# Performance work log

Hardware: AMD Instinct MI355X
Metric: run time of the kernel (lower is better)

## Reference

```python
import jax, jax.numpy as jnp
import numpy as np


def setup_inputs() -> dict:
    key = jax.random.key(0)
    k1, k2, k3 = jax.random.split(key, 3)
    return {
        "x": jax.random.normal(k1, (1, 64, 28, 28), dtype=jnp.float32),
        "w1": jax.random.normal(k2, (128, 32, 3, 3, 2), dtype=jnp.float32),  # weights[0]
        "w2": jax.random.normal(k3, (64, 3, 2), dtype=jnp.float32),          # weights[1]
    }


def reference(x, w1, w2):
    # Stage 1: first unfold + einsum == depthwise size-3 conv along W (pad 1),
    # producing 2 taps (k) per channel.
    xr = x.reshape(64, 28, 28)                      # (j, m=H, n=W)
    xp = jnp.pad(xr, ((0, 0), (0, 0), (1, 1)))      # zero-pad W by 1
    # t3[j, m, i, n] = xp[j, m, n + i]  (i = kernel offset 0..2)
    t3 = jnp.stack([xp[:, :, i:i + 28] for i in range(3)], axis=2)  # (64,28,3,28)
    t4 = jnp.einsum('jmin,jik->jmnk', t3, w2)       # (64,28,28,2)

    # Stage 2: pairwise channel-sum 64 -> 32
    t5 = t4.reshape(32, 2, 28, 28, 2).sum(axis=1)   # (l=32, h=28, w=28, k=2)

    # Stage 3: the two remaining unfolds + final einsum == standard 3x3 conv,
    # pad 1, in_channels = (l,k) = 64, out_channels = 128.
    inp = jnp.transpose(t5, (0, 3, 1, 2)).reshape(1, 64, 28, 28)       # NCHW, C=(l,k)
    w = jnp.transpose(w1, (0, 1, 4, 2, 3)).reshape(128, 64, 3, 3)      # OIHW, I=(l,m)
    y = jax.lax.conv_general_dilated(
        inp, w, window_strides=(1, 1), padding=((1, 1), (1, 1)),
        dimension_numbers=('NCHW', 'OIHW', 'NCHW'))
    return y  # (1, 128, 28, 28)
```

## Files before the change

kernel.cpp:

```cpp
#include <hip/hip_runtime.h>
#include <hip/hip_bf16.h>

__global__ __launch_bounds__(256) void fused_kernel(
    const float* __restrict__ x,
    const float* __restrict__ w1,
    const float* __restrict__ w2,
    float* __restrict__ y)
{
    __shared__ __align__(16) float sA[64 * 6 * 36];
    __shared__ __align__(16) float sRed[256][4];

    const int b     = blockIdx.x;
    const int opair = b / 7;
    const int band  = b % 7;
    const int tid   = threadIdx.x;

    #pragma unroll
    for (int round = 0; round < 2; ++round) {
        int pair = tid + round * 256;
        if (pair < 384) {
            int c  = pair / 6;
            int pr = pair % 6;
            int m  = band * 4 + pr - 1;
            float* dst = &sA[pair * 36];
            if (m < 0 || m > 27) {
                #pragma unroll
                for (int t = 0; t < 15; ++t)
                    ((float2*)dst)[t] = make_float2(0.f, 0.f);
            } else {
                int j0 = c & ~1;
                int k  = c & 1;
                const float* xr0 = x + (j0 * 28 + m) * 28;
                const float* xr1 = xr0 + 28 * 28;
                const float* w2p = w2 + j0 * 6 + k;
                float wa0 = w2p[0], wa1 = w2p[2],  wa2 = w2p[4];
                float wb0 = w2p[6], wb1 = w2p[8],  wb2 = w2p[10];

                float xp0[30], xp1[30];
                xp0[0] = 0.f; xp0[29] = 0.f;
                xp1[0] = 0.f; xp1[29] = 0.f;
                #pragma unroll
                for (int t = 0; t < 7; ++t) {
                    float4 v0 = ((const float4*)xr0)[t];
                    float4 v1 = ((const float4*)xr1)[t];
                    xp0[1 + 4*t] = v0.x; xp0[2 + 4*t] = v0.y;
                    xp0[3 + 4*t] = v0.z; xp0[4 + 4*t] = v0.w;
                    xp1[1 + 4*t] = v1.x; xp1[2 + 4*t] = v1.y;
                    xp1[3 + 4*t] = v1.z; xp1[4 + 4*t] = v1.w;
                }
                float val[30];
                val[0] = 0.f; val[29] = 0.f;
                #pragma unroll
                for (int px = 1; px <= 28; ++px) {
                    val[px] = wa0 * xp0[px-1] + wa1 * xp0[px] + wa2 * xp0[px+1]
                            + wb0 * xp1[px-1] + wb1 * xp1[px] + wb2 * xp1[px+1];
                }
                #pragma unroll
                for (int t = 0; t < 15; ++t)
                    ((float2*)dst)[t] = make_float2(val[2*t], val[2*t + 1]);
            }
        }
    }
    __syncthreads();

    const int oo    = tid >> 7;
    const int r     = tid & 127;
    const int strip = r >> 2;
    const int c4    = r & 3;
    const bool act  = (strip < 28);
    const int dh    = strip / 7;
    const int st    = strip % 7;
    const int o     = opair * 2 + oo;

    float acc0 = 0.f, acc1 = 0.f, acc2 = 0.f, acc3 = 0.f;
    if (act) {
        const float* wbo = w1 + o * 576;
        #pragma unroll 2
        for (int ci = 0; ci < 16; ++ci) {
            int c = c4 + ci * 4;
            const float* wc = wbo + (c >> 1) * 18 + (c & 1);
            const float* sa = &sA[c * 216 + st * 4];
            #pragma unroll
            for (int dy = 0; dy < 3; ++dy) {
                float w0 = wc[dy*6 + 0];
                float w1v = wc[dy*6 + 2];
                float w2v = wc[dy*6 + 4];
                const float* row = sa + (dh + dy) * 36;
                float4 t0 = *(const float4*)row;
                float2 t1 = *(const float2*)(row + 4);
                acc0 += w0 * t0.x + w1v * t0.y + w2v * t0.z;
                acc1 += w0 * t0.y + w1v * t0.z + w2v * t0.w;
                acc2 += w0 * t0.z + w1v * t0.w + w2v * t1.x;
                acc3 += w0 * t0.w + w1v * t1.x + w2v * t1.y;
            }
        }
    }
    sRed[tid][0] = acc0; sRed[tid][1] = acc1;
    sRed[tid][2] = acc2; sRed[tid][3] = acc3;
    __syncthreads();

    if (tid < 224) {
        int oo2 = tid / 112;
        int rr  = tid % 112;
        int dh2 = rr / 28;
        int col = rr % 28;
        int st2 = col >> 2, q = col & 3;
        int base = oo2 * 128 + (dh2 * 7 + st2) * 4;
        float s = sRed[base][q] + sRed[base + 1][q]
                + sRed[base + 2][q] + sRed[base + 3][q];
        int o2 = opair * 2 + oo2;
        int R  = band * 4 + dh2;
        y[(o2 * 28 + R) * 28 + col] = s;
    }
}

extern "C" void kernel_launch(void* const* d_in, const int* in_sizes, int n_in,
                              void* d_out, int out_size, void* d_ws, size_t ws_size,
                              hipStream_t stream) {
    const float* x  = (const float*)d_in[0];
    const float* w1 = (const float*)d_in[1];
    const float* w2 = (const float*)d_in[2];
    float* yout = (float*)d_out;

    fused_kernel<<<dim3(448), dim3(256), 0, stream>>>(x, w1, w2, yout);
}
```

Measured before the change: 16.51 us.

## Halve row band per block, split channels 8-way, reduce via shuffles

Each block now covers a 2-row output band instead of 4, which doubles the grid to 896 blocks, and each output strip is split across 8 channel groups instead of 4. The stage-1 depthwise conv is restructured so each thread computes one padded row with a streaming float4 sliding window, which avoids the large register arrays. The shared-memory partial-sum buffer and its second barrier are replaced by wave shuffles (xor 1, 2, 4), and the output is written as float4. The launch-bounds hint is raised to 4 blocks per CU. The cost is more redundant recomputation of the stage-1 halo rows across blocks, since each block now recomputes 4 rows to produce 2.

```diff
diff --git a/kernel.cpp b/kernel.cpp
--- a/kernel.cpp
+++ b/kernel.cpp
@@ -1,73 +1,69 @@
 #include <hip/hip_runtime.h>
 #include <hip/hip_bf16.h>
 
-__global__ __launch_bounds__(256) void fused_kernel(
+__global__ __launch_bounds__(256, 4) void fused_kernel(
     const float* __restrict__ x,
     const float* __restrict__ w1,
     const float* __restrict__ w2,
     float* __restrict__ y)
 {
-    __shared__ __align__(16) float sA[64 * 6 * 36];
-    __shared__ __align__(16) float sRed[256][4];
+    __shared__ __align__(16) float sA[64 * 148];
 
     const int b     = blockIdx.x;
-    const int opair = b / 7;
-    const int band  = b % 7;
+    const int opair = b / 14;
+    const int band  = b % 14;
     const int tid   = threadIdx.x;
 
-    #pragma unroll
-    for (int round = 0; round < 2; ++round) {
-        int pair = tid + round * 256;
-        if (pair < 384) {
-            int c  = pair / 6;
-            int pr = pair % 6;
-            int m  = band * 4 + pr - 1;
-            float* dst = &sA[pair * 36];
-            if (m < 0 || m > 27) {
-                #pragma unroll
-                for (int t = 0; t < 15; ++t)
-                    ((float2*)dst)[t] = make_float2(0.f, 0.f);
-            } else {
-                int j0 = c & ~1;
-                int k  = c & 1;
-                const float* xr0 = x + (j0 * 28 + m) * 28;
-                const float* xr1 = xr0 + 28 * 28;
-                const float* w2p = w2 + j0 * 6 + k;
-                float wa0 = w2p[0], wa1 = w2p[2],  wa2 = w2p[4];
-                float wb0 = w2p[6], wb1 = w2p[8],  wb2 = w2p[10];
+    {
+        const int c  = tid >> 2;
+        const int pr = tid & 3;
+        const int m  = band * 2 + pr - 1;
+        float* dst = &sA[c * 148 + pr * 36];
+        if (m < 0 || m > 27) {
+            #pragma unroll
+            for (int t = 0; t < 7; ++t)
+                ((float4*)dst)[t] = make_float4(0.f, 0.f, 0.f, 0.f);
+            ((float2*)dst)[14] = make_float2(0.f, 0.f);
+        } else {
+            const int j0 = c & ~1;
+            const int k  = c & 1;
+            const float* xr0 = x + (j0 * 28 + m) * 28;
+            const float* xr1 = xr0 + 28 * 28;
+            const float* w2p = w2 + j0 * 6 + k;
+            const float wa0 = w2p[0], wa1 = w2p[2],  wa2 = w2p[4];
+            const float wb0 = w2p[6], wb1 = w2p[8],  wb2 = w2p[10];
 
-                float xp0[30], xp1[30];
-                xp0[0] = 0.f; xp0[29] = 0.f;
-                xp1[0] = 0.f; xp1[29] = 0.f;
-                #pragma unroll
-                for (int t = 0; t < 7; ++t) {
-                    float4 v0 = ((const float4*)xr0)[t];
-                    float4 v1 = ((const float4*)xr1)[t];
-                    xp0[1 + 4*t] = v0.x; xp0[2 + 4*t] = v0.y;
-                    xp0[3 + 4*t] = v0.z; xp0[4 + 4*t] = v0.w;
-                    xp1[1 + 4*t] = v1.x; xp1[2 + 4*t] = v1.y;
-                    xp1[3 + 4*t] = v1.z; xp1[4 + 4*t] = v1.w;
-                }
-                float val[30];
-                val[0] = 0.f; val[29] = 0.f;
-                #pragma unroll
-                for (int px = 1; px <= 28; ++px) {
-                    val[px] = wa0 * xp0[px-1] + wa1 * xp0[px] + wa2 * xp0[px+1]
-                            + wb0 * xp1[px-1] + wb1 * xp1[px] + wb2 * xp1[px+1];
-                }
-                #pragma unroll
-                for (int t = 0; t < 15; ++t)
-                    ((float2*)dst)[t] = make_float2(val[2*t], val[2*t + 1]);
+            float4 pv0 = make_float4(0.f, 0.f, 0.f, 0.f);
+            float4 pv1 = make_float4(0.f, 0.f, 0.f, 0.f);
+            #pragma unroll
+            for (int t = 0; t < 7; ++t) {
+                float4 v0 = ((const float4*)xr0)[t];
+                float4 v1 = ((const float4*)xr1)[t];
+                float4 o;
+                o.x = wa0 * pv0.z + wa1 * pv0.w + wa2 * v0.x
+                    + wb0 * pv1.z + wb1 * pv1.w + wb2 * v1.x;
+                o.y = wa0 * pv0.w + wa1 * v0.x + wa2 * v0.y
+                    + wb0 * pv1.w + wb1 * v1.x + wb2 * v1.y;
+                o.z = wa0 * v0.x + wa1 * v0.y + wa2 * v0.z
+                    + wb0 * v1.x + wb1 * v1.y + wb2 * v1.z;
+                o.w = wa0 * v0.y + wa1 * v0.z + wa2 * v0.w
+                    + wb0 * v1.y + wb1 * v1.z + wb2 * v1.w;
+                if (t == 0) o.x = 0.f;
+                ((float4*)dst)[t] = o;
+                pv0 = v0; pv1 = v1;
             }
+            float t28 = wa0 * pv0.z + wa1 * pv0.w
+                      + wb0 * pv1.z + wb1 * pv1.w;
+            ((float2*)dst)[14] = make_float2(t28, 0.f);
         }
     }
     __syncthreads();
 
     const int oo    = tid >> 7;
     const int r     = tid & 127;
-    const int strip = r >> 2;
-    const int c4    = r & 3;
-    const bool act  = (strip < 28);
+    const int c8    = r & 7;
+    const int strip = r >> 3;
+    const bool act  = (strip < 14);
     const int dh    = strip / 7;
     const int st    = strip % 7;
     const int o     = opair * 2 + oo;
@@ -76,15 +72,15 @@
     if (act) {
         const float* wbo = w1 + o * 576;
         #pragma unroll 2
-        for (int ci = 0; ci < 16; ++ci) {
-            int c = c4 + ci * 4;
+        for (int ci = 0; ci < 8; ++ci) {
+            const int c = c8 + ci * 8;
             const float* wc = wbo + (c >> 1) * 18 + (c & 1);
-            const float* sa = &sA[c * 216 + st * 4];
+            const float* sa = &sA[c * 148 + st * 4];
             #pragma unroll
             for (int dy = 0; dy < 3; ++dy) {
-                float w0 = wc[dy*6 + 0];
-                float w1v = wc[dy*6 + 2];
-                float w2v = wc[dy*6 + 4];
+                const float w0  = wc[dy * 6 + 0];
+                const float w1v = wc[dy * 6 + 2];
+                const float w2v = wc[dy * 6 + 4];
                 const float* row = sa + (dh + dy) * 36;
                 float4 t0 = *(const float4*)row;
                 float2 t1 = *(const float2*)(row + 4);
@@ -95,22 +91,19 @@
             }
         }
     }
-    sRed[tid][0] = acc0; sRed[tid][1] = acc1;
-    sRed[tid][2] = acc2; sRed[tid][3] = acc3;
-    __syncthreads();
 
-    if (tid < 224) {
-        int oo2 = tid / 112;
-        int rr  = tid % 112;
-        int dh2 = rr / 28;
-        int col = rr % 28;
-        int st2 = col >> 2, q = col & 3;
-        int base = oo2 * 128 + (dh2 * 7 + st2) * 4;
-        float s = sRed[base][q] + sRed[base + 1][q]
-                + sRed[base + 2][q] + sRed[base + 3][q];
-        int o2 = opair * 2 + oo2;
-        int R  = band * 4 + dh2;
-        y[(o2 * 28 + R) * 28 + col] = s;
+    #pragma unroll
+    for (int m = 1; m <= 4; m <<= 1) {
+        acc0 += __shfl_xor(acc0, m);
+        acc1 += __shfl_xor(acc1, m);
+        acc2 += __shfl_xor(acc2, m);
+        acc3 += __shfl_xor(acc3, m);
+    }
+
+    if (act && c8 == 0) {
+        const int R = band * 2 + dh;
+        float* yp = y + (o * 28 + R) * 28 + st * 4;
+        *(float4*)yp = make_float4(acc0, acc1, acc2, acc3);
     }
 }
 
@@ -122,5 +115,5 @@
     const float* w2 = (const float*)d_in[2];
     float* yout = (float*)d_out;
 
-    fused_kernel<<<dim3(448), dim3(256), 0, stream>>>(x, w1, w2, yout);
+    fused_kernel<<<dim3(896), dim3(256), 0, stream>>>(x, w1, w2, yout);
 }
```

Measured after the change: 17.34 us. +5.0%, slower.
